# Optimization experiments

Measured on AMD Instinct MI355X. Metric: run time of the kernel, lower is better.

The kernel has to match this reference:

```python
import jax, jax.numpy as jnp
import numpy as np

N = 20000   # nodes
E = 160000  # edges
C = 512     # input_size / channels
D = 16      # edge_size
H = 256     # hidden_size
EPS = 1e-5  # BatchNorm eps (eval mode, init running stats: mean=0, var=1)


def setup_inputs() -> dict:
    key = jax.random.key(0)
    ks = jax.random.split(key, 24)
    w = lambda k, shape: (jax.random.normal(k, shape, jnp.float32) * 0.02)
    inp = {
        "x": jax.random.normal(ks[0], (N, C), jnp.float32),
        "edge_index": jax.random.randint(ks[1], (2, E), 0, N, jnp.int32),
        "edge_attr": jax.random.normal(ks[2], (E, D), jnp.float32),
        "goal_feat": jax.random.normal(ks[3], (N, C), jnp.float32),
        # CGConv 1
        "Wf1": w(ks[4], (2 * C + D, C)), "bf1": jnp.zeros((C,), jnp.float32),
        "Ws1": w(ks[5], (2 * C + D, C)), "bs1": jnp.zeros((C,), jnp.float32),
        "g1": jnp.ones((C,), jnp.float32), "be1": jnp.zeros((C,), jnp.float32),
        # CGConv 2
        "Wf2": w(ks[6], (2 * C + D, C)), "bf2": jnp.zeros((C,), jnp.float32),
        "Ws2": w(ks[7], (2 * C + D, C)), "bs2": jnp.zeros((C,), jnp.float32),
        "g2": jnp.ones((C,), jnp.float32), "be2": jnp.zeros((C,), jnp.float32),
        # GCNConv 3, 4
        "W3": w(ks[8], (C, H)), "b3": jnp.zeros((H,), jnp.float32),
        "W4": w(ks[9], (H, H)), "b4": jnp.zeros((H,), jnp.float32),
        # distance MLP: Lin(H+C -> C), ReLU, Lin(C -> 1)
        "Wd1": w(ks[10], (H + C, C)), "bd1": jnp.zeros((C,), jnp.float32),
        "Wd2": w(ks[11], (C, 1)), "bd2": jnp.zeros((1,), jnp.float32),
    }
    return inp


def cg_conv(x, src, dst, edge_attr, Wf, bf, Ws, bs, gamma, beta):
    # PyG CGConv: z = x_i || x_j || e;  m = sigmoid(lin_f(z)) * softplus(lin_s(z))
    # aggr='add' at targets, BatchNorm (eval, init stats), residual.
    z = jnp.concatenate([x[dst], x[src], edge_attr], axis=-1)  # [E, 2C+D]
    m = jax.nn.sigmoid(z @ Wf + bf) * jax.nn.softplus(z @ Ws + bs)  # [E, C]
    agg = jax.ops.segment_sum(m, dst, num_segments=N)  # [N, C]
    agg = agg * (gamma / jnp.sqrt(1.0 + EPS)) + beta   # BN eval (mean=0, var=1)
    return agg + x


def gcn_conv(x, src, dst, W, b):
    # PyG GCNConv with add_self_loops=True, normalize=True
    h = x @ W  # [N, out]
    loop = jnp.arange(N, dtype=src.dtype)
    s = jnp.concatenate([src, loop])
    d = jnp.concatenate([dst, loop])
    deg = jax.ops.segment_sum(jnp.ones_like(d, jnp.float32), d, num_segments=N)
    dinv = jnp.where(deg > 0, jax.lax.rsqrt(jnp.maximum(deg, 1.0)), 0.0)
    norm = dinv[s] * dinv[d]  # [E+N]
    out = jax.ops.segment_sum(norm[:, None] * h[s], d, num_segments=N)
    return out + b


def reference(x, edge_index, edge_attr, goal_feat,
              Wf1, bf1, Ws1, bs1, g1, be1,
              Wf2, bf2, Ws2, bs2, g2, be2,
              W3, b3, W4, b4, Wd1, bd1, Wd2, bd2):
    src = edge_index[0]  # x_j (source)
    dst = edge_index[1]  # x_i (target)
    h = jax.nn.relu(cg_conv(x, src, dst, edge_attr, Wf1, bf1, Ws1, bs1, g1, be1))
    h = jax.nn.relu(cg_conv(h, src, dst, edge_attr, Wf2, bf2, Ws2, bs2, g2, be2))
    h = jax.nn.relu(gcn_conv(h, src, dst, W3, b3))
    h = jax.nn.relu(gcn_conv(h, src, dst, W4, b4))
    z = jnp.concatenate([h, goal_feat], axis=1)  # [N, H+C]
    pred_dist = jax.nn.relu(z @ Wd1 + bd1) @ Wd2 + bd2  # [N, 1]
    return pred_dist, h
```

## Files before the change

kernel.cpp:

```cpp
#include <hip/hip_runtime.h>
#include <stdint.h>

#define NNODES 20000
#define NEDGES 160000
#define NPAD   20096

typedef float f32x4 __attribute__((ext_vector_type(4)));
typedef float f32x2 __attribute__((ext_vector_type(2)));
typedef short s16x8 __attribute__((ext_vector_type(8)));

__device__ __forceinline__ float b2f(unsigned short b) {
    unsigned int u = ((unsigned int)b) << 16;
    return __builtin_bit_cast(float, u);
}
__device__ __forceinline__ unsigned short f2b(float f) {
    unsigned int u = __builtin_bit_cast(unsigned int, f);
    unsigned int r = (u + 0x7FFFu + ((u >> 16) & 1u)) >> 16;
    return (unsigned short)r;
}
__device__ __forceinline__ f32x2 unpack2(unsigned int u) {
    f32x2 r;
    r.x = __builtin_bit_cast(float, u << 16);
    r.y = __builtin_bit_cast(float, u & 0xFFFF0000u);
    return r;
}

__global__ __launch_bounds__(256) void gemm_bt_kernel(
    const unsigned short* __restrict__ A,
    const unsigned short* __restrict__ BT,
    float* __restrict__ Cf,
    unsigned short* __restrict__ Cb,
    int M, int N, int K,
    const float* __restrict__ bias)
{
    __shared__ unsigned short As[128 * 32];
    __shared__ unsigned short Bs[128 * 32];
    const int tid  = threadIdx.x;
    const int wid  = tid >> 6;
    const int lane = tid & 63;
    const int bm = blockIdx.x * 128;
    const int bn = blockIdx.y * 128;
    const int wm = (wid & 1) * 64;
    const int wn = (wid >> 1) * 64;

    f32x4 acc[4][4];
#pragma unroll
    for (int i = 0; i < 4; i++)
#pragma unroll
        for (int j = 0; j < 4; j++) acc[i][j] = {0.f, 0.f, 0.f, 0.f};

    for (int k0 = 0; k0 < K; k0 += 32) {
#pragma unroll
        for (int r = 0; r < 2; r++) {
            int flat = r * 256 + tid;
            int row  = flat >> 2;
            int part = flat & 3;
            const unsigned short* ga = A  + (size_t)(bm + row) * K + k0 + part * 8;
            const unsigned short* gb = BT + (size_t)(bn + row) * K + k0 + part * 8;
            __builtin_amdgcn_global_load_lds(
                (const __attribute__((address_space(1))) unsigned int*)ga,
                (__attribute__((address_space(3))) unsigned int*)&As[flat * 8], 16, 0, 0);
            __builtin_amdgcn_global_load_lds(
                (const __attribute__((address_space(1))) unsigned int*)gb,
                (__attribute__((address_space(3))) unsigned int*)&Bs[flat * 8], 16, 0, 0);
        }
        __syncthreads();

        const int kq = (lane >> 4) * 8;
        const int rl = lane & 15;
        s16x8 af[4], bfr[4];
#pragma unroll
        for (int mi = 0; mi < 4; mi++)
            af[mi] = *(const s16x8*)&As[(wm + mi * 16 + rl) * 32 + kq];
#pragma unroll
        for (int ni = 0; ni < 4; ni++)
            bfr[ni] = *(const s16x8*)&Bs[(wn + ni * 16 + rl) * 32 + kq];
#pragma unroll
        for (int mi = 0; mi < 4; mi++)
#pragma unroll
            for (int ni = 0; ni < 4; ni++)
                acc[mi][ni] = __builtin_amdgcn_mfma_f32_16x16x32_bf16(
                    af[mi], bfr[ni], acc[mi][ni], 0, 0, 0);
        __syncthreads();
    }

    const int cl = lane & 15;
    const int rq = (lane >> 4) * 4;
#pragma unroll
    for (int mi = 0; mi < 4; mi++)
#pragma unroll
        for (int ni = 0; ni < 4; ni++)
#pragma unroll
            for (int r = 0; r < 4; r++) {
                int row = bm + wm + mi * 16 + rq + r;
                int col = bn + wn + ni * 16 + cl;
                float v = acc[mi][ni][r];
                if (Cb) {
                    if (bias) v = fmaxf(v + bias[col], 0.f);
                    Cb[(size_t)row * N + col] = f2b(v);
                } else {
                    Cf[(size_t)row * N + col] = v;
                }
            }
}

__global__ void count_kernel(const int* __restrict__ ei, int* __restrict__ counts) {
    int e = blockIdx.x * blockDim.x + threadIdx.x;
    if (e < NEDGES) atomicAdd(&counts[ei[NEDGES + e]], 1);
}

__global__ __launch_bounds__(1024) void scan_kernel(const int* __restrict__ counts,
                                                    int* __restrict__ row_ptr)
{
    __shared__ int sdata[1024];
    const int t = threadIdx.x;
    int vals[20];
    const int base = t * 20;
    int lsum = 0;
#pragma unroll
    for (int j = 0; j < 20; j++) {
        int idx = base + j;
        int v = (idx < NNODES) ? counts[idx] : 0;
        vals[j] = v; lsum += v;
    }
    sdata[t] = lsum;
    __syncthreads();
    for (int off = 1; off < 1024; off <<= 1) {
        int v = (t >= off) ? sdata[t - off] : 0;
        __syncthreads();
        sdata[t] += v;
        __syncthreads();
    }
    int run = sdata[t] - lsum;
#pragma unroll
    for (int j = 0; j < 20; j++) {
        int idx = base + j;
        if (idx < NNODES) row_ptr[idx] = run;
        run += vals[j];
    }
    if (t == 1023) row_ptr[NNODES] = sdata[1023];
}

__global__ void fill_kernel(const int* __restrict__ ei,
                            const int* __restrict__ row_ptr,
                            int* __restrict__ cursor,
                            int2* __restrict__ csr)
{
    int e = blockIdx.x * blockDim.x + threadIdx.x;
    if (e >= NEDGES) return;
    int dst = ei[NEDGES + e];
    int p = row_ptr[dst] + atomicAdd(&cursor[dst], 1);
    csr[p] = make_int2(ei[e], e);
}

__global__ void dinv_kernel(const int* __restrict__ row_ptr, float* __restrict__ dinv) {
    int i = blockIdx.x * blockDim.x + threadIdx.x;
    if (i < NNODES) {
        int deg = row_ptr[i + 1] - row_ptr[i] + 1;
        dinv[i] = rsqrtf((float)deg);
    }
}

__global__ void pad_copy_kernel(const float* __restrict__ src,
                                unsigned short* __restrict__ dst,
                                int valid_rows, int cols, long total)
{
    long idx = (long)blockIdx.x * blockDim.x + threadIdx.x;
    if (idx >= total) return;
    int n = (int)(idx / cols);
    dst[idx] = (n < valid_rows) ? f2b(src[idx]) : (unsigned short)0;
}

__global__ void pack_cgw_kernel(const float* __restrict__ Wf,
                                const float* __restrict__ Ws,
                                unsigned short* __restrict__ out)
{
    int idx = blockIdx.x * blockDim.x + threadIdx.x;
    if (idx >= 2048 * 512) return;
    int j = idx >> 9;
    int k = idx & 511;
    int half = (j >= 1024);
    int jj = j & 1023;
    int c  = (jj >> 2) * 2 + (jj & 1);
    int fs = (jj >> 1) & 1;
    const float* W = fs ? Ws : Wf;
    float v = W[(size_t)(half ? 512 + k : k) * 512 + c];
    out[idx] = f2b(v);
}

__global__ void pack_t_kernel(const float* __restrict__ W,
                              unsigned short* __restrict__ WT,
                              int K, int Nout)
{
    long idx = (long)blockIdx.x * blockDim.x + threadIdx.x;
    if (idx >= (long)K * Nout) return;
    int j = (int)(idx / K);
    int k = (int)(idx % K);
    WT[idx] = f2b(W[(size_t)k * Nout + j]);
}

#define CG_NPB 4
__global__ __launch_bounds__(256, 1) void cg_gather_kernel(
    const unsigned short* __restrict__ P,
    const int* __restrict__ row_ptr,
    const int2* __restrict__ csr,
    const float* __restrict__ ea,
    const float* __restrict__ Wf,
    const float* __restrict__ Ws,
    const float* __restrict__ bfv,
    const float* __restrict__ bsv,
    const float* __restrict__ g,
    const float* __restrict__ be,
    const float* __restrict__ xresf,
    const unsigned short* __restrict__ xresb,
    unsigned short* __restrict__ hout)
{
    const int tid = threadIdx.x;
    const int c0  = tid * 2;
    const int nbase = blockIdx.x * CG_NPB;

    f32x2 wf[16], wsv[16];
#pragma unroll
    for (int k = 0; k < 16; k++) {
        const size_t rb = (size_t)(1024 + k) * 512;
        wf[k]  = *(const f32x2*)&Wf[rb + c0];
        wsv[k] = *(const f32x2*)&Ws[rb + c0];
    }
    const f32x2 bfx = *(const f32x2*)&bfv[c0];
    const f32x2 bsx = *(const f32x2*)&bsv[c0];
    const f32x2 gv  = *(const f32x2*)&g[c0];
    const f32x2 bev = *(const f32x2*)&be[c0];
    const float rs = rsqrtf(1.f + 1e-5f);

    for (int n = nbase; n < nbase + CG_NPB; n++) {
        if (n >= NNODES) {
            *(unsigned int*)&hout[(size_t)n * 512 + c0] = 0;
            continue;
        }
        const unsigned short* Pd = P + (size_t)n * 2048;
        const uint2 qb = *(const uint2*)(Pd + c0 * 2);
        const f32x2 baseF = unpack2(qb.x) + bfx;
        const f32x2 baseS = unpack2(qb.y) + bsx;

        f32x2 acc = {0.f, 0.f};
        const int i0 = row_ptr[n], i1 = row_ptr[n + 1];

        if (i0 < i1) {
            int2 se = csr[i0];
            int sx = __builtin_amdgcn_readfirstlane(se.x);
            int sy = __builtin_amdgcn_readfirstlane(se.y);
            const float4* ep = (const float4*)(ea + (size_t)sy * 16);
            float4 e0 = ep[0], e1 = ep[1], e2 = ep[2], e3 = ep[3];
            uint2 q = *(const uint2*)(P + (size_t)sx * 2048 + 1024 + c0 * 2);

            for (int i = i0; i < i1; i++) {
                float4 c0v = e0, c1v = e1, c2v = e2, c3v = e3;
                uint2  cq  = q;
                if (i + 1 < i1) {
                    int2 se2 = csr[i + 1];
                    int sx2 = __builtin_amdgcn_readfirstlane(se2.x);
                    int sy2 = __builtin_amdgcn_readfirstlane(se2.y);
                    const float4* ep2 = (const float4*)(ea + (size_t)sy2 * 16);
                    e0 = ep2[0]; e1 = ep2[1]; e2 = ep2[2]; e3 = ep2[3];
                    q = *(const uint2*)(P + (size_t)sx2 * 2048 + 1024 + c0 * 2);
                }
                f32x2 f = baseF + unpack2(cq.x);
                f32x2 s = baseS + unpack2(cq.y);
                const float ek[16] = {c0v.x, c0v.y, c0v.z, c0v.w,
                                      c1v.x, c1v.y, c1v.z, c1v.w,
                                      c2v.x, c2v.y, c2v.z, c2v.w,
                                      c3v.x, c3v.y, c3v.z, c3v.w};
#pragma unroll
                for (int k = 0; k < 16; k++) {
                    f32x2 ev = {ek[k], ek[k]};
                    f = __builtin_elementwise_fma(ev, wf[k], f);
                    s = __builtin_elementwise_fma(ev, wsv[k], s);
                }
                float sp0 = __logf(1.f + __expf(s.x));
                float sp1 = __logf(1.f + __expf(s.y));
                float sg0 = __builtin_amdgcn_rcpf(1.f + __expf(-f.x));
                float sg1 = __builtin_amdgcn_rcpf(1.f + __expf(-f.y));
                acc.x = fmaf(sp0, sg0, acc.x);
                acc.y = fmaf(sp1, sg1, acc.y);
            }
        }
        f32x2 res;
        if (xresf) {
            res = *(const f32x2*)&xresf[(size_t)n * 512 + c0];
        } else {
            res = unpack2(*(const unsigned int*)&xresb[(size_t)n * 512 + c0]);
        }
        float v0 = fmaxf(acc.x * (gv.x * rs) + bev.x + res.x, 0.f);
        float v1 = fmaxf(acc.y * (gv.y * rs) + bev.y + res.y, 0.f);
        unsigned int packed = (unsigned int)f2b(v0) | ((unsigned int)f2b(v1) << 16);
        *(unsigned int*)&hout[(size_t)n * 512 + c0] = packed;
    }
}

__global__ __launch_bounds__(256) void gcn_gather_kernel(
    const unsigned short* __restrict__ pre,
    const int* __restrict__ row_ptr,
    const int2* __restrict__ csr,
    const float* __restrict__ dinv,
    const float* __restrict__ b,
    unsigned short* __restrict__ hout,
    float* __restrict__ doutf)
{
    const int tid = threadIdx.x;
    const int n = blockIdx.x * 2 + (tid >> 7);
    const int c = (tid & 127) * 2;
    if (n >= NNODES) {
        if (n < NPAD) *(unsigned int*)&hout[(size_t)n * 256 + c] = 0;
        return;
    }
    const float din = dinv[n];
    f32x2 acc = {0.f, 0.f};
    const int i0 = row_ptr[n], i1 = row_ptr[n + 1];
    if (i0 < i1) {
        int sx = __builtin_amdgcn_readfirstlane(csr[i0].x);
        float dv = dinv[sx];
        unsigned int pv = *(const unsigned int*)&pre[(size_t)sx * 256 + c];
        for (int i = i0; i < i1; i++) {
            float cdv = dv; unsigned int cpv = pv;
            if (i + 1 < i1) {
                int sx2 = __builtin_amdgcn_readfirstlane(csr[i + 1].x);
                dv = dinv[sx2];
                pv = *(const unsigned int*)&pre[(size_t)sx2 * 256 + c];
            }
            f32x2 p = unpack2(cpv);
            acc.x = fmaf(cdv, p.x, acc.x);
            acc.y = fmaf(cdv, p.y, acc.y);
        }
    }
    f32x2 self = unpack2(*(const unsigned int*)&pre[(size_t)n * 256 + c]);
    const f32x2 bv = *(const f32x2*)&b[c];
    float v0 = fmaxf(fmaf(acc.x, din, din * din * self.x) + bv.x, 0.f);
    float v1 = fmaxf(fmaf(acc.y, din, din * din * self.y) + bv.y, 0.f);
    *(unsigned int*)&hout[(size_t)n * 256 + c] =
        (unsigned int)f2b(v0) | ((unsigned int)f2b(v1) << 16);
    if (doutf) {
        f32x2 vv = {v0, v1};
        *(f32x2*)&doutf[(size_t)n * 256 + c] = vv;
    }
}

__global__ void build_zc_kernel(const unsigned short* __restrict__ h4,
                                const float* __restrict__ goal,
                                unsigned short* __restrict__ zc)
{
    long idx = (long)blockIdx.x * blockDim.x + threadIdx.x;
    if (idx >= (long)NPAD * 768) return;
    int n = (int)(idx / 768);
    int c = (int)(idx % 768);
    unsigned short v = 0;
    if (n < NNODES)
        v = (c < 256) ? h4[(size_t)n * 256 + c]
                      : f2b(goal[(size_t)n * 512 + (c - 256)]);
    zc[idx] = v;
}

__global__ __launch_bounds__(256) void final_dot_kernel(
    const unsigned short* __restrict__ t,
    const float* __restrict__ Wd2,
    const float* __restrict__ bd2,
    float* __restrict__ pred)
{
    const int lane = threadIdx.x & 63;
    const int wid  = threadIdx.x >> 6;
    float w[8];
#pragma unroll
    for (int i = 0; i < 8; i++) w[i] = Wd2[lane * 8 + i];
    const float bd = bd2[0];
    for (int n = blockIdx.x * 4 + wid; n < NNODES; n += gridDim.x * 4) {
        const unsigned short* tp = t + (size_t)n * 512 + lane * 8;
        float s = 0.f;
#pragma unroll
        for (int i = 0; i < 8; i++) s = fmaf(b2f(tp[i]), w[i], s);
#pragma unroll
        for (int off = 32; off; off >>= 1) s += __shfl_xor(s, off, 64);
        if (lane == 0) pred[n] = s + bd;
    }
}

extern "C" void kernel_launch(void* const* d_in, const int* in_sizes, int n_in,
                              void* d_out, int out_size, void* d_ws, size_t ws_size,
                              hipStream_t stream)
{
    (void)in_sizes; (void)n_in; (void)out_size; (void)ws_size;
    const float* x    = (const float*)d_in[0];
    const int*   ei   = (const int*)d_in[1];
    const float* ea   = (const float*)d_in[2];
    const float* goal = (const float*)d_in[3];
    const float* Wf1  = (const float*)d_in[4];
    const float* bf1  = (const float*)d_in[5];
    const float* Ws1  = (const float*)d_in[6];
    const float* bs1  = (const float*)d_in[7];
    const float* g1   = (const float*)d_in[8];
    const float* be1  = (const float*)d_in[9];
    const float* Wf2  = (const float*)d_in[10];
    const float* bf2  = (const float*)d_in[11];
    const float* Ws2  = (const float*)d_in[12];
    const float* bs2  = (const float*)d_in[13];
    const float* g2   = (const float*)d_in[14];
    const float* be2  = (const float*)d_in[15];
    const float* W3   = (const float*)d_in[16];
    const float* b3   = (const float*)d_in[17];
    const float* W4   = (const float*)d_in[18];
    const float* b4   = (const float*)d_in[19];
    const float* Wd1  = (const float*)d_in[20];
    const float* bd1  = (const float*)d_in[21];
    const float* Wd2  = (const float*)d_in[22];
    const float* bd2  = (const float*)d_in[23];
    float* outp = (float*)d_out;

    char* ws = (char*)d_ws;
    size_t off = 0;
    auto alloc = [&](size_t bytes) -> char* {
        char* p = ws + off;
        off += (bytes + 255) & ~(size_t)255;
        return p;
    };
    unsigned short* P     = (unsigned short*)alloc((size_t)NPAD * 2048 * 2);
    unsigned short* bufA  = (unsigned short*)alloc((size_t)NPAD * 512 * 2);
    unsigned short* bufB  = (unsigned short*)alloc((size_t)NPAD * 512 * 2);
    unsigned short* bufC  = (unsigned short*)alloc((size_t)NPAD * 512 * 2);
    unsigned short* wpack = (unsigned short*)alloc((size_t)2048 * 512 * 2);
    int*            counts  = (int*)alloc((size_t)NNODES * 4);
    int*            row_ptr = (int*)alloc((size_t)(NNODES + 1) * 4);
    int2*           csr     = (int2*)alloc((size_t)NEDGES * 8);
    float*          dinv    = (float*)alloc((size_t)NNODES * 4);

    unsigned short* xpad  = bufA;
    unsigned short* h1    = bufB;
    unsigned short* h2    = bufA;
    unsigned short* pre_b = bufB;
    unsigned short* h3    = bufC;
    unsigned short* h4    = bufA;
    unsigned short* zc    = P;
    unsigned short* tb    = P + (size_t)NPAD * 1024;

    const int B = 256;

    hipMemsetAsync(counts, 0, (size_t)NNODES * 4, stream);
    count_kernel<<<(NEDGES + B - 1) / B, B, 0, stream>>>(ei, counts);
    scan_kernel<<<1, 1024, 0, stream>>>(counts, row_ptr);
    hipMemsetAsync(counts, 0, (size_t)NNODES * 4, stream);
    fill_kernel<<<(NEDGES + B - 1) / B, B, 0, stream>>>(ei, row_ptr, counts, csr);
    dinv_kernel<<<(NNODES + B - 1) / B, B, 0, stream>>>(row_ptr, dinv);

    {
        long tot = (long)NPAD * 512;
        pad_copy_kernel<<<(unsigned)((tot + B - 1) / B), B, 0, stream>>>(x, xpad, NNODES, 512, tot);
    }

    dim3 gBig(NPAD / 128, 2048 / 128);

    pack_cgw_kernel<<<(2048 * 512 + B - 1) / B, B, 0, stream>>>(Wf1, Ws1, wpack);
    gemm_bt_kernel<<<gBig, B, 0, stream>>>(xpad, wpack, nullptr, P, NPAD, 2048, 512, nullptr);
    cg_gather_kernel<<<NPAD / CG_NPB, B, 0, stream>>>(P, row_ptr, csr, ea,
                                                      Wf1, Ws1, bf1, bs1, g1, be1,
                                                      x, nullptr, h1);

    pack_cgw_kernel<<<(2048 * 512 + B - 1) / B, B, 0, stream>>>(Wf2, Ws2, wpack);
    gemm_bt_kernel<<<gBig, B, 0, stream>>>(h1, wpack, nullptr, P, NPAD, 2048, 512, nullptr);
    cg_gather_kernel<<<NPAD / CG_NPB, B, 0, stream>>>(P, row_ptr, csr, ea,
                                                      Wf2, Ws2, bf2, bs2, g2, be2,
                                                      nullptr, h1, h2);

    pack_t_kernel<<<(256 * 512 + B - 1) / B, B, 0, stream>>>(W3, wpack, 512, 256);
    gemm_bt_kernel<<<dim3(NPAD / 128, 2), B, 0, stream>>>(h2, wpack, nullptr, pre_b, NPAD, 256, 512, nullptr);
    gcn_gather_kernel<<<NPAD / 2, B, 0, stream>>>(pre_b, row_ptr, csr, dinv, b3, h3, (float*)nullptr);

    pack_t_kernel<<<(256 * 256 + B - 1) / B, B, 0, stream>>>(W4, wpack, 256, 256);
    gemm_bt_kernel<<<dim3(NPAD / 128, 2), B, 0, stream>>>(h3, wpack, nullptr, pre_b, NPAD, 256, 256, nullptr);
    gcn_gather_kernel<<<NPAD / 2, B, 0, stream>>>(pre_b, row_ptr, csr, dinv, b4, h4, outp + NNODES);

    build_zc_kernel<<<(unsigned)(((long)NPAD * 768 + B - 1) / B), B, 0, stream>>>(h4, goal, zc);
    pack_t_kernel<<<(512 * 768 + B - 1) / B, B, 0, stream>>>(Wd1, wpack, 768, 512);
    gemm_bt_kernel<<<dim3(NPAD / 128, 4), B, 0, stream>>>(zc, wpack, nullptr, tb, NPAD, 512, 768, bd1);
    final_dot_kernel<<<512, B, 0, stream>>>(tb, Wd2, bd2, outp);
}
```

Baseline: 825.8 us.

## Use fp16 dot2 for CGConv edge-feature projection with CSR-ordered packed edge attrs

Edge attributes are pre-packed into fp16 pairs in CSR order, and the edge-weight rows are packed into fp16 pairs, so the per-edge 16-wide projection uses v_dot2_f32_f16 instead of 32 fp32 FMAs per channel pair. The packing also makes edge-attribute reads contiguous instead of gathered by edge id. The explicit software prefetch is replaced by a 2-way unrolled loop. It costs fp16 rounding of edge features and weights plus a one-time pack kernel.

```diff
diff --git a/kernel.cpp b/kernel.cpp
--- a/kernel.cpp
+++ b/kernel.cpp
@@ -8,6 +8,8 @@
 typedef float f32x4 __attribute__((ext_vector_type(4)));
 typedef float f32x2 __attribute__((ext_vector_type(2)));
 typedef short s16x8 __attribute__((ext_vector_type(8)));
+typedef unsigned int u32x4 __attribute__((ext_vector_type(4)));
+typedef _Float16 h16x2 __attribute__((ext_vector_type(2)));
 
 __device__ __forceinline__ float b2f(unsigned short b) {
     unsigned int u = ((unsigned int)b) << 16;
@@ -23,6 +25,20 @@
     r.x = __builtin_bit_cast(float, u << 16);
     r.y = __builtin_bit_cast(float, u & 0xFFFF0000u);
     return r;
+}
+__device__ __forceinline__ unsigned int packh2(float a, float b) {
+    h16x2 h = { (_Float16)a, (_Float16)b };
+    return __builtin_bit_cast(unsigned int, h);
+}
+__device__ __forceinline__ float dot2h(unsigned int a, unsigned int b, float c) {
+#if __has_builtin(__builtin_amdgcn_fdot2)
+    return __builtin_amdgcn_fdot2(__builtin_bit_cast(h16x2, a),
+                                  __builtin_bit_cast(h16x2, b), c, false);
+#else
+    float d;
+    asm("v_dot2_f32_f16 %0, %1, %2, %3" : "=v"(d) : "v"(a), "v"(b), "v"(c));
+    return d;
+#endif
 }
 
 __global__ __launch_bounds__(256) void gemm_bt_kernel(
@@ -199,14 +215,41 @@
     WT[idx] = f2b(W[(size_t)k * Nout + j]);
 }
 
+__global__ void pack_we_kernel(const float* __restrict__ Wf,
+                               const float* __restrict__ Ws,
+                               unsigned int* __restrict__ out)
+{
+    int idx = blockIdx.x * blockDim.x + threadIdx.x;
+    if (idx >= 8192) return;
+    int q  = idx & 3;
+    int c2 = (idx >> 2) & 255;
+    int k  = idx >> 10;
+    const float* W = (q >> 1) ? Ws : Wf;
+    int c = c2 * 2 + (q & 1);
+    float v0 = W[(size_t)(1024 + 2 * k) * 512 + c];
+    float v1 = W[(size_t)(1024 + 2 * k + 1) * 512 + c];
+    out[idx] = packh2(v0, v1);
+}
+
+__global__ void pack_ea_kernel(const int2* __restrict__ csr,
+                               const float* __restrict__ ea,
+                               unsigned int* __restrict__ out)
+{
+    int idx = blockIdx.x * blockDim.x + threadIdx.x;
+    if (idx >= NEDGES * 8) return;
+    int i = idx >> 3;
+    int j = idx & 7;
+    int eid = csr[i].y;
+    out[idx] = packh2(ea[(size_t)eid * 16 + 2 * j], ea[(size_t)eid * 16 + 2 * j + 1]);
+}
+
 #define CG_NPB 4
 __global__ __launch_bounds__(256, 1) void cg_gather_kernel(
     const unsigned short* __restrict__ P,
     const int* __restrict__ row_ptr,
     const int2* __restrict__ csr,
-    const float* __restrict__ ea,
-    const float* __restrict__ Wf,
-    const float* __restrict__ Ws,
+    const u32x4* __restrict__ wE,
+    const u32x4* __restrict__ eapk,
     const float* __restrict__ bfv,
     const float* __restrict__ bsv,
     const float* __restrict__ g,
@@ -219,13 +262,10 @@
     const int c0  = tid * 2;
     const int nbase = blockIdx.x * CG_NPB;
 
-    f32x2 wf[16], wsv[16];
-#pragma unroll
-    for (int k = 0; k < 16; k++) {
-        const size_t rb = (size_t)(1024 + k) * 512;
-        wf[k]  = *(const f32x2*)&Wf[rb + c0];
-        wsv[k] = *(const f32x2*)&Ws[rb + c0];
-    }
+    u32x4 w[8];
+#pragma unroll
+    for (int k = 0; k < 8; k++) w[k] = wE[k * 256 + tid];
+
     const f32x2 bfx = *(const f32x2*)&bfv[c0];
     const f32x2 bsx = *(const f32x2*)&bsv[c0];
     const f32x2 gv  = *(const f32x2*)&g[c0];
@@ -245,45 +285,44 @@
         f32x2 acc = {0.f, 0.f};
         const int i0 = row_ptr[n], i1 = row_ptr[n + 1];
 
-        if (i0 < i1) {
-            int2 se = csr[i0];
-            int sx = __builtin_amdgcn_readfirstlane(se.x);
-            int sy = __builtin_amdgcn_readfirstlane(se.y);
-            const float4* ep = (const float4*)(ea + (size_t)sy * 16);
-            float4 e0 = ep[0], e1 = ep[1], e2 = ep[2], e3 = ep[3];
+        auto do_edge = [&](int i) {
+            const int sx = __builtin_amdgcn_readfirstlane(csr[i].x);
+            u32x4 a0 = eapk[(size_t)i * 2];
+            u32x4 a1 = eapk[(size_t)i * 2 + 1];
             uint2 q = *(const uint2*)(P + (size_t)sx * 2048 + 1024 + c0 * 2);
-
-            for (int i = i0; i < i1; i++) {
-                float4 c0v = e0, c1v = e1, c2v = e2, c3v = e3;
-                uint2  cq  = q;
-                if (i + 1 < i1) {
-                    int2 se2 = csr[i + 1];
-                    int sx2 = __builtin_amdgcn_readfirstlane(se2.x);
-                    int sy2 = __builtin_amdgcn_readfirstlane(se2.y);
-                    const float4* ep2 = (const float4*)(ea + (size_t)sy2 * 16);
-                    e0 = ep2[0]; e1 = ep2[1]; e2 = ep2[2]; e3 = ep2[3];
-                    q = *(const uint2*)(P + (size_t)sx2 * 2048 + 1024 + c0 * 2);
-                }
-                f32x2 f = baseF + unpack2(cq.x);
-                f32x2 s = baseS + unpack2(cq.y);
-                const float ek[16] = {c0v.x, c0v.y, c0v.z, c0v.w,
-                                      c1v.x, c1v.y, c1v.z, c1v.w,
-                                      c2v.x, c2v.y, c2v.z, c2v.w,
-                                      c3v.x, c3v.y, c3v.z, c3v.w};
-#pragma unroll
-                for (int k = 0; k < 16; k++) {
-                    f32x2 ev = {ek[k], ek[k]};
-                    f = __builtin_elementwise_fma(ev, wf[k], f);
-                    s = __builtin_elementwise_fma(ev, wsv[k], s);
-                }
-                float sp0 = __logf(1.f + __expf(s.x));
-                float sp1 = __logf(1.f + __expf(s.y));
-                float sg0 = __builtin_amdgcn_rcpf(1.f + __expf(-f.x));
-                float sg1 = __builtin_amdgcn_rcpf(1.f + __expf(-f.y));
-                acc.x = fmaf(sp0, sg0, acc.x);
-                acc.y = fmaf(sp1, sg1, acc.y);
+            float f0 = baseF.x, f1 = baseF.y, s0 = baseS.x, s1 = baseS.y;
+#pragma unroll
+            for (int k = 0; k < 4; k++) {
+                f0 = dot2h(a0[k], w[k][0], f0);
+                f1 = dot2h(a0[k], w[k][1], f1);
+                s0 = dot2h(a0[k], w[k][2], s0);
+                s1 = dot2h(a0[k], w[k][3], s1);
             }
+#pragma unroll
+            for (int k = 0; k < 4; k++) {
+                f0 = dot2h(a1[k], w[4 + k][0], f0);
+                f1 = dot2h(a1[k], w[4 + k][1], f1);
+                s0 = dot2h(a1[k], w[4 + k][2], s0);
+                s1 = dot2h(a1[k], w[4 + k][3], s1);
+            }
+            f32x2 pf = unpack2(q.x);
+            f32x2 ps = unpack2(q.y);
+            f0 += pf.x; f1 += pf.y; s0 += ps.x; s1 += ps.y;
+            float sp0 = __logf(1.f + __expf(s0));
+            float sp1 = __logf(1.f + __expf(s1));
+            float sg0 = __builtin_amdgcn_rcpf(1.f + __expf(-f0));
+            float sg1 = __builtin_amdgcn_rcpf(1.f + __expf(-f1));
+            acc.x = fmaf(sp0, sg0, acc.x);
+            acc.y = fmaf(sp1, sg1, acc.y);
+        };
+
+        int i = i0;
+        for (; i + 1 < i1; i += 2) {
+            do_edge(i);
+            do_edge(i + 1);
         }
+        if (i < i1) do_edge(i);
+
         f32x2 res;
         if (xresf) {
             res = *(const f32x2*)&xresf[(size_t)n * 512 + c0];
@@ -429,6 +468,8 @@
     int*            row_ptr = (int*)alloc((size_t)(NNODES + 1) * 4);
     int2*           csr     = (int2*)alloc((size_t)NEDGES * 8);
     float*          dinv    = (float*)alloc((size_t)NNODES * 4);
+    unsigned int*   wEbuf   = (unsigned int*)alloc((size_t)8192 * 4);
+    unsigned int*   eapk    = (unsigned int*)alloc((size_t)NEDGES * 8 * 4);
 
     unsigned short* xpad  = bufA;
     unsigned short* h1    = bufB;
@@ -447,6 +488,7 @@
     hipMemsetAsync(counts, 0, (size_t)NNODES * 4, stream);
     fill_kernel<<<(NEDGES + B - 1) / B, B, 0, stream>>>(ei, row_ptr, counts, csr);
     dinv_kernel<<<(NNODES + B - 1) / B, B, 0, stream>>>(row_ptr, dinv);
+    pack_ea_kernel<<<(NEDGES * 8 + B - 1) / B, B, 0, stream>>>(csr, ea, eapk);
 
     {
         long tot = (long)NPAD * 512;
@@ -456,15 +498,19 @@
     dim3 gBig(NPAD / 128, 2048 / 128);
 
     pack_cgw_kernel<<<(2048 * 512 + B - 1) / B, B, 0, stream>>>(Wf1, Ws1, wpack);
+    pack_we_kernel<<<(8192 + B - 1) / B, B, 0, stream>>>(Wf1, Ws1, wEbuf);
     gemm_bt_kernel<<<gBig, B, 0, stream>>>(xpad, wpack, nullptr, P, NPAD, 2048, 512, nullptr);
-    cg_gather_kernel<<<NPAD / CG_NPB, B, 0, stream>>>(P, row_ptr, csr, ea,
-                                                      Wf1, Ws1, bf1, bs1, g1, be1,
+    cg_gather_kernel<<<NPAD / CG_NPB, B, 0, stream>>>(P, row_ptr, csr,
+                                                      (const u32x4*)wEbuf, (const u32x4*)eapk,
+                                                      bf1, bs1, g1, be1,
                                                       x, nullptr, h1);
 
     pack_cgw_kernel<<<(2048 * 512 + B - 1) / B, B, 0, stream>>>(Wf2, Ws2, wpack);
     gemm_bt_kernel<<<gBig, B, 0, stream>>>(h1, wpack, nullptr, P, NPAD, 2048, 512, nullptr);
-    cg_gather_kernel<<<NPAD / CG_NPB, B, 0, stream>>>(P, row_ptr, csr, ea,
-                                                      Wf2, Ws2, bf2, bs2, g2, be2,
+    pack_we_kernel<<<(8192 + B - 1) / B, B, 0, stream>>>(Wf2, Ws2, wEbuf);
+    cg_gather_kernel<<<NPAD / CG_NPB, B, 0, stream>>>(P, row_ptr, csr,
+                                                      (const u32x4*)wEbuf, (const u32x4*)eapk,
+                                                      bf2, bs2, g2, be2,
                                                       nullptr, h1, h2);
 
     pack_t_kernel<<<(256 * 512 + B - 1) / B, B, 0, stream>>>(W3, wpack, 512, 256);
```

Result: no change. 821.4 us (-0.5%).
